# Performance work log

Hardware: AMD Instinct MI355X
Metric: run time of the kernel (lower is better)

## Reference

```python
import jax, jax.numpy as jnp
import numpy as np

U, I, K = 20000, 10000, 64
HID = [128, 64, 32, 16]  # hidden[0] must equal 2*K
B = 4096


def _lin(key, out_f, in_f):
    # torch nn.Linear default init ~ U(-1/sqrt(in), 1/sqrt(in)); normal/sqrt(in) is fine for a baseline
    return jax.random.normal(key, (out_f, in_f), jnp.float32) / np.sqrt(in_f)


def setup_inputs() -> dict:
    key = jax.random.key(0)
    ks = jax.random.split(key, 12)
    # near-binary implicit-feedback interaction matrix [U+1, I+1]
    interactions = (jax.random.uniform(ks[0], (U + 1, I + 1)) < 0.05).astype(jnp.float32)
    user_idx = jax.random.randint(ks[1], (B,), 0, U)
    item_idx = jax.random.randint(ks[2], (B,), 0, I)
    W_u = _lin(ks[3], K, I)   # proj_u: Linear(n_items -> K, bias=False)
    W_i = _lin(ks[4], K, U)   # proj_i: Linear(n_users -> K, bias=False)
    inp = dict(interactions=interactions, user_idx=user_idx, item_idx=item_idx,
               W_u=W_u, W_i=W_i)
    # matching_fn: 3 blocks of Linear + LayerNorm (+ReLU, dropout=0 in eval)
    for j in range(1, len(HID)):
        inp[f'W{j}'] = _lin(ks[4 + j], HID[j], HID[j - 1])
        inp[f'b{j}'] = jnp.zeros((HID[j],), jnp.float32)
        inp[f'g{j}'] = jnp.ones((HID[j],), jnp.float32)
        inp[f'be{j}'] = jnp.zeros((HID[j],), jnp.float32)
    inp['Wp'] = _lin(ks[8], 1, HID[-1])
    inp['bp'] = jnp.zeros((1,), jnp.float32)
    return inp


def _layernorm(x, g, b, eps=1e-5):
    m = jnp.mean(x, axis=-1, keepdims=True)
    v = jnp.mean(jnp.square(x - m), axis=-1, keepdims=True)
    return (x - m) * jax.lax.rsqrt(v + eps) * g + b


def reference(interactions, user_idx, item_idx, W_u, W_i,
              W1, b1, g1, be1, W2, b2, g2, be2, W3, b3, g3, be3, Wp, bp):
    rows = jnp.arange(user_idx.shape[0])
    # gather user history rows [B, I], zero-mask the target item
    u_slice = interactions[user_idx, :-1].at[rows, item_idx].set(0.0)
    # gather item history rows [B, U], zero-mask the target user
    i_slice = interactions.T[item_idx, :-1].at[rows, user_idx].set(0.0)
    u_emb = u_slice @ W_u.T  # [B, K]
    i_emb = i_slice @ W_i.T  # [B, K]
    x = jnp.concatenate([u_emb, i_emb], axis=-1)  # [B, 2K]
    for (W, b, g, be) in ((W1, b1, g1, be1), (W2, b2, g2, be2), (W3, b3, g3, be3)):
        x = jax.nn.relu(_layernorm(x @ W.T + b, g, be))
    logit = jnp.squeeze(x @ Wp.T + bp, -1)  # [B]
    return logit
```

## Files before the change

kernel.cpp:

```cpp
#include <hip/hip_runtime.h>

#define U_ROWS 20000
#define I_COLS 10000
#define LDI    10001
#define B_N    4096
#define SU     313
#define SC     625

typedef __attribute__((ext_vector_type(8))) __bf16 bf16x8;
typedef __attribute__((ext_vector_type(4))) float f32x4;

__device__ __forceinline__ unsigned short f2bf(float f) {
    unsigned int u = __float_as_uint(f);
    return (unsigned short)((u + 0x7FFFu + ((u >> 16) & 1u)) >> 16);
}

__global__ __launch_bounds__(256) void k_pack_w(const float* __restrict__ W,
                                                unsigned short* __restrict__ out,
                                                int n_k, int n_steps)
{
    int idx = blockIdx.x * blockDim.x + threadIdx.x;
    if (idx >= n_steps * 2048) return;
    int j  = idx & 7;
    int l  = (idx >> 3) & 63;
    int nb = (idx >> 9) & 3;
    int s  = idx >> 11;
    int n  = nb * 16 + (l & 15);
    int k  = s * 32 + ((l >> 4) << 3) + j;
    float v = (k < n_k) ? W[(size_t)n * n_k + k] : 0.0f;
    out[idx] = f2bf(v);
}

__global__ __launch_bounds__(256) void k_tr(const float* __restrict__ in,
                                            float* __restrict__ out, int rows, int cols)
{
    int idx = blockIdx.x * blockDim.x + threadIdx.x;
    if (idx >= rows * cols) return;
    int r = idx / cols, c = idx % cols;
    out[c * rows + r] = in[idx];
}

__global__ __launch_bounds__(256) void k_gemm_u(
    const float* __restrict__ A, const int* __restrict__ uidx,
    const unsigned short* __restrict__ Bp, float* __restrict__ Upart,
    int steps_per)
{
    __shared__ float At[64 * 32];
    const int t = threadIdx.x, lane = t & 63, w = t >> 6;
    const int mb = blockIdx.x & 63, p = blockIdx.x >> 6;
    const int r0 = mb * 64;
    const int s0 = p * steps_per;
    const int s1 = (SU < s0 + steps_per) ? SU : (s0 + steps_per);
    const int rl = lane & 15, g = lane >> 4;

    f32x4 acc[4];
#pragma unroll
    for (int nb = 0; nb < 4; ++nb) acc[nb] = (f32x4)(0.0f);

    int urow[8];
#pragma unroll
    for (int q = 0; q < 8; ++q) urow[q] = uidx[r0 + q * 8 + (t >> 5)];

    for (int s = s0; s < s1; ++s) {
        const int k0 = s * 32;
        float sv[8];
#pragma unroll
        for (int q = 0; q < 8; ++q) {
            int row = q * 8 + (t >> 5);
            int col = k0 + (((t & 31) + row) & 31);
            sv[q] = (col < I_COLS) ? A[(size_t)urow[q] * LDI + col] : 0.0f;
        }
        __syncthreads();
#pragma unroll
        for (int q = 0; q < 8; ++q) {
            int row = q * 8 + (t >> 5);
            At[row * 32 + (t & 31)] = sv[q];
        }
        __syncthreads();

        bf16x8 bv[4];
#pragma unroll
        for (int nb = 0; nb < 4; ++nb)
            bv[nb] = *(const bf16x8*)(Bp + ((size_t)(s * 4 + nb) * 64 + lane) * 8);

        const int r_loc = w * 16 + rl;
        unsigned int au[8];
#pragma unroll
        for (int j = 0; j < 8; ++j) {
            int c = g * 8 + j;
            au[j] = __float_as_uint(At[r_loc * 32 + ((c - r_loc) & 31)]);
        }
        union { int i[4]; bf16x8 v; } af;
#pragma unroll
        for (int q = 0; q < 4; ++q)
            af.i[q] = __builtin_amdgcn_perm(au[2 * q + 1], au[2 * q], 0x07060302);
#pragma unroll
        for (int nb = 0; nb < 4; ++nb)
            acc[nb] = __builtin_amdgcn_mfma_f32_16x16x32_bf16(af.v, bv[nb], acc[nb], 0, 0, 0);
    }

    float* outp = Upart + (size_t)p * B_N * 64;
#pragma unroll
    for (int nb = 0; nb < 4; ++nb)
#pragma unroll
        for (int reg = 0; reg < 4; ++reg) {
            int r = r0 + w * 16 + g * 4 + reg;
            outp[(size_t)r * 64 + nb * 16 + rl] = acc[nb][reg];
        }
}

__global__ __launch_bounds__(256) void k_gemm_c(
    const float* __restrict__ A, const unsigned short* __restrict__ Bp,
    float* __restrict__ Cpart, int n_mb, int steps_per)
{
    __shared__ float At[32 * 64];
    const int t = threadIdx.x, lane = t & 63, w = t >> 6;
    const int mb = blockIdx.x % n_mb, p = blockIdx.x / n_mb;
    const int i0 = mb * 64;
    const int s0 = p * steps_per;
    const int s1 = (SC < s0 + steps_per) ? SC : (s0 + steps_per);
    const int rl = lane & 15, g = lane >> 4;

    f32x4 acc[4];
#pragma unroll
    for (int nb = 0; nb < 4; ++nb) acc[nb] = (f32x4)(0.0f);

    for (int s = s0; s < s1; ++s) {
        const int u0 = s * 32;
        float sv[8];
#pragma unroll
        for (int q = 0; q < 8; ++q) {
            int ul = q * 4 + w;
            int col = i0 + ((lane + ul) & 63);
            sv[q] = (col < I_COLS) ? A[(size_t)(u0 + ul) * LDI + col] : 0.0f;
        }
        __syncthreads();
#pragma unroll
        for (int q = 0; q < 8; ++q) At[(q * 4 + w) * 64 + lane] = sv[q];
        __syncthreads();

        bf16x8 bv[4];
#pragma unroll
        for (int nb = 0; nb < 4; ++nb)
            bv[nb] = *(const bf16x8*)(Bp + ((size_t)(s * 4 + nb) * 64 + lane) * 8);

        const int i_loc = w * 16 + rl;
        unsigned int au[8];
#pragma unroll
        for (int j = 0; j < 8; ++j) {
            int ul = g * 8 + j;
            au[j] = __float_as_uint(At[ul * 64 + ((i_loc - ul) & 63)]);
        }
        union { int i[4]; bf16x8 v; } af;
#pragma unroll
        for (int q = 0; q < 4; ++q)
            af.i[q] = __builtin_amdgcn_perm(au[2 * q + 1], au[2 * q], 0x07060302);
#pragma unroll
        for (int nb = 0; nb < 4; ++nb)
            acc[nb] = __builtin_amdgcn_mfma_f32_16x16x32_bf16(af.v, bv[nb], acc[nb], 0, 0, 0);
    }

    float* outp = Cpart + (size_t)p * I_COLS * 64;
#pragma unroll
    for (int nb = 0; nb < 4; ++nb)
#pragma unroll
        for (int reg = 0; reg < 4; ++reg) {
            int i = i0 + w * 16 + g * 4 + reg;
            if (i < I_COLS) outp[(size_t)i * 64 + nb * 16 + rl] = acc[nb][reg];
        }
}

__device__ __forceinline__ float redsum64(float x) {
    x += __shfl_xor(x, 1);  x += __shfl_xor(x, 2);  x += __shfl_xor(x, 4);
    x += __shfl_xor(x, 8);  x += __shfl_xor(x, 16); x += __shfl_xor(x, 32);
    return x;
}
__device__ __forceinline__ float redsum32(float x) {
    x += __shfl_xor(x, 1); x += __shfl_xor(x, 2); x += __shfl_xor(x, 4);
    x += __shfl_xor(x, 8); x += __shfl_xor(x, 16);
    return x;
}
__device__ __forceinline__ float redsum16(float x) {
    x += __shfl_xor(x, 1); x += __shfl_xor(x, 2); x += __shfl_xor(x, 4);
    x += __shfl_xor(x, 8);
    return x;
}

__global__ __launch_bounds__(256) void k_epi(
    const float* __restrict__ A, const int* __restrict__ uidx, const int* __restrict__ iidx,
    const float* __restrict__ Upart, const float* __restrict__ Cpart, int NP, int NC,
    const float* __restrict__ Wu, const float* __restrict__ Wi,
    const float* __restrict__ Wt1, const float* __restrict__ b1, const float* __restrict__ g1, const float* __restrict__ be1,
    const float* __restrict__ Wt2, const float* __restrict__ b2, const float* __restrict__ g2, const float* __restrict__ be2,
    const float* __restrict__ Wt3, const float* __restrict__ b3, const float* __restrict__ g3, const float* __restrict__ be3,
    const float* __restrict__ Wp, const float* __restrict__ bp,
    float* __restrict__ out)
{
    const int t = threadIdx.x, lane = t & 63, w = t >> 6;
    const int r = blockIdx.x * 4 + w;
    const int u = uidx[r], it = iidx[r];
    const float a_ui = A[(size_t)u * LDI + it];

    float ue = 0.f, ie = 0.f;
    for (int p0 = 0; p0 < NP; ++p0) ue += Upart[((size_t)p0 * B_N + r) * 64 + lane];
    for (int p0 = 0; p0 < NC; ++p0) ie += Cpart[((size_t)p0 * I_COLS + it) * 64 + lane];
    ue -= a_ui * Wu[(size_t)lane * I_COLS + it];
    ie -= a_ui * Wi[(size_t)lane * U_ROWS + u];

    float h = b1[lane];
    for (int c = 0; c < 64; ++c) h += __shfl(ue, c) * Wt1[c * 64 + lane];
    for (int c = 0; c < 64; ++c) h += __shfl(ie, c) * Wt1[(64 + c) * 64 + lane];
    {
        float m = redsum64(h) * (1.0f / 64.0f);
        float d = h - m;
        float v = redsum64(d * d) * (1.0f / 64.0f);
        h = d * rsqrtf(v + 1e-5f) * g1[lane] + be1[lane];
        h = fmaxf(h, 0.0f);
    }
    const int l2 = lane & 31;
    float h2 = b2[l2];
    for (int c = 0; c < 64; ++c) h2 += __shfl(h, c) * Wt2[c * 32 + l2];
    {
        float m = redsum32(h2) * (1.0f / 32.0f);
        float d = h2 - m;
        float v = redsum32(d * d) * (1.0f / 32.0f);
        h2 = d * rsqrtf(v + 1e-5f) * g2[l2] + be2[l2];
        h2 = fmaxf(h2, 0.0f);
    }
    const int l3 = lane & 15;
    float h3 = b3[l3];
    for (int c = 0; c < 32; ++c) h3 += __shfl(h2, c) * Wt3[c * 16 + l3];
    {
        float m = redsum16(h3) * (1.0f / 16.0f);
        float d = h3 - m;
        float v = redsum16(d * d) * (1.0f / 16.0f);
        h3 = d * rsqrtf(v + 1e-5f) * g3[l3] + be3[l3];
        h3 = fmaxf(h3, 0.0f);
    }
    float tt = h3 * Wp[l3];
    tt = redsum16(tt);
    if (lane == 0) out[r] = tt + bp[0];
}

extern "C" void kernel_launch(void* const* d_in, const int* in_sizes, int n_in,
                              void* d_out, int out_size, void* d_ws, size_t ws_size,
                              hipStream_t stream)
{
    const float* A    = (const float*)d_in[0];
    const int*   uidx = (const int*)d_in[1];
    const int*   iidx = (const int*)d_in[2];
    const float* W_u  = (const float*)d_in[3];
    const float* W_i  = (const float*)d_in[4];
    const float* W1   = (const float*)d_in[5];
    const float* b1   = (const float*)d_in[6];
    const float* g1   = (const float*)d_in[7];
    const float* be1  = (const float*)d_in[8];
    const float* W2   = (const float*)d_in[9];
    const float* b2   = (const float*)d_in[10];
    const float* g2   = (const float*)d_in[11];
    const float* be2  = (const float*)d_in[12];
    const float* W3   = (const float*)d_in[13];
    const float* b3   = (const float*)d_in[14];
    const float* g3   = (const float*)d_in[15];
    const float* be3  = (const float*)d_in[16];
    const float* Wp   = (const float*)d_in[17];
    const float* bp   = (const float*)d_in[18];
    float* out = (float*)d_out;

    unsigned short* Wtu_p = (unsigned short*)d_ws;
    unsigned short* Wti_p = Wtu_p + (size_t)SU * 2048;
    float* Wt1 = (float*)(Wti_p + (size_t)SC * 2048);
    float* Wt2 = Wt1 + 128 * 64;
    float* Wt3 = Wt2 + 64 * 32;
    float* Upart = Wt3 + 32 * 16;

    size_t fixed_b = (size_t)(SU + SC) * 2048 * 2 + (size_t)(128 * 64 + 64 * 32 + 32 * 16) * 4;
    int NP = 8, NC = 8;
    while (NP > 1 &&
           fixed_b + (size_t)NP * B_N * 64 * 4 + (size_t)NC * I_COLS * 64 * 4 > ws_size) {
        NP >>= 1; NC >>= 1;
    }
    float* Cpart = Upart + (size_t)NP * B_N * 64;

    int spu = (SU + NP - 1) / NP;
    int spc = (SC + NC - 1) / NC;

    hipLaunchKernelGGL(k_pack_w, dim3((SU * 2048 + 255) / 256), dim3(256), 0, stream,
                       W_u, Wtu_p, I_COLS, SU);
    hipLaunchKernelGGL(k_pack_w, dim3((SC * 2048 + 255) / 256), dim3(256), 0, stream,
                       W_i, Wti_p, U_ROWS, SC);
    hipLaunchKernelGGL(k_tr, dim3(32), dim3(256), 0, stream, W1, Wt1, 64, 128);
    hipLaunchKernelGGL(k_tr, dim3(8),  dim3(256), 0, stream, W2, Wt2, 32, 64);
    hipLaunchKernelGGL(k_tr, dim3(2),  dim3(256), 0, stream, W3, Wt3, 16, 32);

    hipLaunchKernelGGL(k_gemm_u, dim3(64 * NP), dim3(256), 0, stream,
                       A, uidx, Wtu_p, Upart, spu);
    hipLaunchKernelGGL(k_gemm_c, dim3(157 * NC), dim3(256), 0, stream,
                       A, Wti_p, Cpart, 157, spc);

    hipLaunchKernelGGL(k_epi, dim3(B_N / 4), dim3(256), 0, stream,
                       A, uidx, iidx, Upart, Cpart, NP, NC,
                       W_u, W_i, Wt1, b1, g1, be1, Wt2, b2, g2, be2,
                       Wt3, b3, g3, be3, Wp, bp, out);
}
```

Measured before the change: 302.0 us.

## Merge prep and GEMM launches, software-pipeline global loads in GEMM loops

Folds the two weight-pack kernels and three transpose kernels into one prep kernel. Merges the user-side and item-side GEMMs into a single launch whose blocks branch by index. Each GEMM loop now prefetches the next step's A tile into registers before writing the current one to shared memory, so global-load latency overlaps the MFMA work. This cuts launch overhead and lets the two GEMMs share the GPU, at the cost of more registers and more divergent code per kernel.

```diff
diff --git a/kernel.cpp b/kernel.cpp
--- a/kernel.cpp
+++ b/kernel.cpp
@@ -15,159 +15,180 @@
     return (unsigned short)((u + 0x7FFFu + ((u >> 16) & 1u)) >> 16);
 }
 
-__global__ __launch_bounds__(256) void k_pack_w(const float* __restrict__ W,
-                                                unsigned short* __restrict__ out,
-                                                int n_k, int n_steps)
+__global__ __launch_bounds__(256) void k_prep(
+    const float* __restrict__ Wu, const float* __restrict__ Wi,
+    unsigned short* __restrict__ Pu, unsigned short* __restrict__ Pi,
+    const float* __restrict__ W1, const float* __restrict__ W2, const float* __restrict__ W3,
+    float* __restrict__ Wt1, float* __restrict__ Wt2, float* __restrict__ Wt3)
 {
-    int idx = blockIdx.x * blockDim.x + threadIdx.x;
-    if (idx >= n_steps * 2048) return;
-    int j  = idx & 7;
-    int l  = (idx >> 3) & 63;
-    int nb = (idx >> 9) & 3;
-    int s  = idx >> 11;
-    int n  = nb * 16 + (l & 15);
-    int k  = s * 32 + ((l >> 4) << 3) + j;
-    float v = (k < n_k) ? W[(size_t)n * n_k + k] : 0.0f;
-    out[idx] = f2bf(v);
-}
-
-__global__ __launch_bounds__(256) void k_tr(const float* __restrict__ in,
-                                            float* __restrict__ out, int rows, int cols)
+    const int NU = SU * 2048, NC2 = SC * 2048;
+    int idx = blockIdx.x * 256 + threadIdx.x;
+    if (idx < NU + NC2) {
+        const float* W = (idx < NU) ? Wu : Wi;
+        unsigned short* out = (idx < NU) ? Pu : Pi;
+        int n_k = (idx < NU) ? I_COLS : U_ROWS;
+        int li = (idx < NU) ? idx : idx - NU;
+        int j  = li & 7;
+        int l  = (li >> 3) & 63;
+        int nb = (li >> 9) & 3;
+        int s  = li >> 11;
+        int n  = nb * 16 + (l & 15);
+        int k  = s * 32 + ((l >> 4) << 3) + j;
+        float v = (k < n_k) ? W[(size_t)n * n_k + k] : 0.0f;
+        out[li] = f2bf(v);
+        return;
+    }
+    int r2 = idx - (NU + NC2);
+    if (r2 < 64 * 128) { int r = r2 / 128, c = r2 % 128; Wt1[c * 64 + r] = W1[r2]; return; }
+    r2 -= 64 * 128;
+    if (r2 < 32 * 64)  { int r = r2 / 64,  c = r2 % 64;  Wt2[c * 32 + r] = W2[r2]; return; }
+    r2 -= 32 * 64;
+    if (r2 < 16 * 32)  { int r = r2 / 32,  c = r2 % 32;  Wt3[c * 16 + r] = W3[r2]; return; }
+}
+
+__global__ __launch_bounds__(256) void k_gemm(
+    const float* __restrict__ A, const int* __restrict__ uidx,
+    const unsigned short* __restrict__ Bpu, const unsigned short* __restrict__ Bpc,
+    float* __restrict__ Upart, float* __restrict__ Cpart,
+    int spu, int spc, int NC)
 {
-    int idx = blockIdx.x * blockDim.x + threadIdx.x;
-    if (idx >= rows * cols) return;
-    int r = idx / cols, c = idx % cols;
-    out[c * rows + r] = in[idx];
-}
-
-__global__ __launch_bounds__(256) void k_gemm_u(
-    const float* __restrict__ A, const int* __restrict__ uidx,
-    const unsigned short* __restrict__ Bp, float* __restrict__ Upart,
-    int steps_per)
-{
-    __shared__ float At[64 * 32];
+    __shared__ float At[2048];
     const int t = threadIdx.x, lane = t & 63, w = t >> 6;
-    const int mb = blockIdx.x & 63, p = blockIdx.x >> 6;
-    const int r0 = mb * 64;
-    const int s0 = p * steps_per;
-    const int s1 = (SU < s0 + steps_per) ? SU : (s0 + steps_per);
     const int rl = lane & 15, g = lane >> 4;
+    const int CB = 157 * NC;
 
     f32x4 acc[4];
 #pragma unroll
     for (int nb = 0; nb < 4; ++nb) acc[nb] = (f32x4)(0.0f);
 
-    int urow[8];
-#pragma unroll
-    for (int q = 0; q < 8; ++q) urow[q] = uidx[r0 + q * 8 + (t >> 5)];
-
-    for (int s = s0; s < s1; ++s) {
-        const int k0 = s * 32;
+    if ((int)blockIdx.x < CB) {
+        const int mb = blockIdx.x % 157, p = blockIdx.x / 157;
+        const int i0 = mb * 64;
+        const int s0 = p * spc;
+        const int s1 = (SC < s0 + spc) ? SC : (s0 + spc);
+
+#define CLOAD(dst, S) do { \
+        int u0_ = (S) * 32; \
+        _Pragma("unroll") \
+        for (int q = 0; q < 8; ++q) { \
+            int ul_ = q * 4 + w; \
+            int col_ = i0 + ((lane + ul_) & 63); \
+            dst[q] = (col_ < I_COLS) ? A[(size_t)(u0_ + ul_) * LDI + col_] : 0.0f; \
+        } } while (0)
+
         float sv[8];
-#pragma unroll
-        for (int q = 0; q < 8; ++q) {
-            int row = q * 8 + (t >> 5);
-            int col = k0 + (((t & 31) + row) & 31);
-            sv[q] = (col < I_COLS) ? A[(size_t)urow[q] * LDI + col] : 0.0f;
+        CLOAD(sv, s0);
+        for (int s = s0; s < s1; ++s) {
+            __syncthreads();
+            float sv2[8];
+            if (s + 1 < s1) { CLOAD(sv2, s + 1); }
+            else {
+#pragma unroll
+                for (int q = 0; q < 8; ++q) sv2[q] = 0.0f;
+            }
+#pragma unroll
+            for (int q = 0; q < 8; ++q) At[(q * 4 + w) * 64 + lane] = sv[q];
+
+            bf16x8 bv[4];
+#pragma unroll
+            for (int nb = 0; nb < 4; ++nb)
+                bv[nb] = *(const bf16x8*)(Bpc + ((size_t)(s * 4 + nb) * 64 + lane) * 8);
+            __syncthreads();
+
+            const int i_loc = w * 16 + rl;
+            unsigned int au[8];
+#pragma unroll
+            for (int j = 0; j < 8; ++j) {
+                int ul = g * 8 + j;
+                au[j] = __float_as_uint(At[ul * 64 + ((i_loc - ul) & 63)]);
+            }
+            union { int i[4]; bf16x8 v; } af;
+#pragma unroll
+            for (int q = 0; q < 4; ++q)
+                af.i[q] = __builtin_amdgcn_perm(au[2 * q + 1], au[2 * q], 0x07060302);
+#pragma unroll
+            for (int nb = 0; nb < 4; ++nb)
+                acc[nb] = __builtin_amdgcn_mfma_f32_16x16x32_bf16(af.v, bv[nb], acc[nb], 0, 0, 0);
+#pragma unroll
+            for (int q = 0; q < 8; ++q) sv[q] = sv2[q];
         }
-        __syncthreads();
-#pragma unroll
-        for (int q = 0; q < 8; ++q) {
-            int row = q * 8 + (t >> 5);
-            At[row * 32 + (t & 31)] = sv[q];
+
+        float* outp = Cpart + (size_t)p * I_COLS * 64;
+#pragma unroll
+        for (int nb = 0; nb < 4; ++nb)
+#pragma unroll
+            for (int reg = 0; reg < 4; ++reg) {
+                int i = i0 + w * 16 + g * 4 + reg;
+                if (i < I_COLS) outp[(size_t)i * 64 + nb * 16 + rl] = acc[nb][reg];
+            }
+    } else {
+        const int bid = blockIdx.x - CB;
+        const int mb = bid & 63, p = bid >> 6;
+        const int r0 = mb * 64;
+        const int s0 = p * spu;
+        const int s1 = (SU < s0 + spu) ? SU : (s0 + spu);
+
+        int urow[8];
+#pragma unroll
+        for (int q = 0; q < 8; ++q) urow[q] = uidx[r0 + q * 8 + (t >> 5)];
+
+#define ULOAD(dst, S) do { \
+        int k0_ = (S) * 32; \
+        _Pragma("unroll") \
+        for (int q = 0; q < 8; ++q) { \
+            int row_ = q * 8 + (t >> 5); \
+            int col_ = k0_ + (((t & 31) + row_) & 31); \
+            dst[q] = (col_ < I_COLS) ? A[(size_t)urow[q] * LDI + col_] : 0.0f; \
+        } } while (0)
+
+        float sv[8];
+        ULOAD(sv, s0);
+        for (int s = s0; s < s1; ++s) {
+            __syncthreads();
+            float sv2[8];
+            if (s + 1 < s1) { ULOAD(sv2, s + 1); }
+            else {
+#pragma unroll
+                for (int q = 0; q < 8; ++q) sv2[q] = 0.0f;
+            }
+#pragma unroll
+            for (int q = 0; q < 8; ++q) {
+                int row = q * 8 + (t >> 5);
+                At[row * 32 + (t & 31)] = sv[q];
+            }
+            bf16x8 bv[4];
+#pragma unroll
+            for (int nb = 0; nb < 4; ++nb)
+                bv[nb] = *(const bf16x8*)(Bpu + ((size_t)(s * 4 + nb) * 64 + lane) * 8);
+            __syncthreads();
+
+            const int r_loc = w * 16 + rl;
+            unsigned int au[8];
+#pragma unroll
+            for (int j = 0; j < 8; ++j) {
+                int c = g * 8 + j;
+                au[j] = __float_as_uint(At[r_loc * 32 + ((c - r_loc) & 31)]);
+            }
+            union { int i[4]; bf16x8 v; } af;
+#pragma unroll
+            for (int q = 0; q < 4; ++q)
+                af.i[q] = __builtin_amdgcn_perm(au[2 * q + 1], au[2 * q], 0x07060302);
+#pragma unroll
+            for (int nb = 0; nb < 4; ++nb)
+                acc[nb] = __builtin_amdgcn_mfma_f32_16x16x32_bf16(af.v, bv[nb], acc[nb], 0, 0, 0);
+#pragma unroll
+            for (int q = 0; q < 8; ++q) sv[q] = sv2[q];
         }
-        __syncthreads();
-
-        bf16x8 bv[4];
+
+        float* outp = Upart + (size_t)p * B_N * 64;
 #pragma unroll
         for (int nb = 0; nb < 4; ++nb)
-            bv[nb] = *(const bf16x8*)(Bp + ((size_t)(s * 4 + nb) * 64 + lane) * 8);
-
-        const int r_loc = w * 16 + rl;
-        unsigned int au[8];
-#pragma unroll
-        for (int j = 0; j < 8; ++j) {
-            int c = g * 8 + j;
-            au[j] = __float_as_uint(At[r_loc * 32 + ((c - r_loc) & 31)]);
-        }
-        union { int i[4]; bf16x8 v; } af;
-#pragma unroll
-        for (int q = 0; q < 4; ++q)
-            af.i[q] = __builtin_amdgcn_perm(au[2 * q + 1], au[2 * q], 0x07060302);
-#pragma unroll
-        for (int nb = 0; nb < 4; ++nb)
-            acc[nb] = __builtin_amdgcn_mfma_f32_16x16x32_bf16(af.v, bv[nb], acc[nb], 0, 0, 0);
-    }
-
-    float* outp = Upart + (size_t)p * B_N * 64;
-#pragma unroll
-    for (int nb = 0; nb < 4; ++nb)
-#pragma unroll
-        for (int reg = 0; reg < 4; ++reg) {
-            int r = r0 + w * 16 + g * 4 + reg;
-            outp[(size_t)r * 64 + nb * 16 + rl] = acc[nb][reg];
-        }
-}
-
-__global__ __launch_bounds__(256) void k_gemm_c(
-    const float* __restrict__ A, const unsigned short* __restrict__ Bp,
-    float* __restrict__ Cpart, int n_mb, int steps_per)
-{
-    __shared__ float At[32 * 64];
-    const int t = threadIdx.x, lane = t & 63, w = t >> 6;
-    const int mb = blockIdx.x % n_mb, p = blockIdx.x / n_mb;
-    const int i0 = mb * 64;
-    const int s0 = p * steps_per;
-    const int s1 = (SC < s0 + steps_per) ? SC : (s0 + steps_per);
-    const int rl = lane & 15, g = lane >> 4;
-
-    f32x4 acc[4];
-#pragma unroll
-    for (int nb = 0; nb < 4; ++nb) acc[nb] = (f32x4)(0.0f);
-
-    for (int s = s0; s < s1; ++s) {
-        const int u0 = s * 32;
-        float sv[8];
-#pragma unroll
-        for (int q = 0; q < 8; ++q) {
-            int ul = q * 4 + w;
-            int col = i0 + ((lane + ul) & 63);
-            sv[q] = (col < I_COLS) ? A[(size_t)(u0 + ul) * LDI + col] : 0.0f;
-        }
-        __syncthreads();
-#pragma unroll
-        for (int q = 0; q < 8; ++q) At[(q * 4 + w) * 64 + lane] = sv[q];
-        __syncthreads();
-
-        bf16x8 bv[4];
-#pragma unroll
-        for (int nb = 0; nb < 4; ++nb)
-            bv[nb] = *(const bf16x8*)(Bp + ((size_t)(s * 4 + nb) * 64 + lane) * 8);
-
-        const int i_loc = w * 16 + rl;
-        unsigned int au[8];
-#pragma unroll
-        for (int j = 0; j < 8; ++j) {
-            int ul = g * 8 + j;
-            au[j] = __float_as_uint(At[ul * 64 + ((i_loc - ul) & 63)]);
-        }
-        union { int i[4]; bf16x8 v; } af;
-#pragma unroll
-        for (int q = 0; q < 4; ++q)
-            af.i[q] = __builtin_amdgcn_perm(au[2 * q + 1], au[2 * q], 0x07060302);
-#pragma unroll
-        for (int nb = 0; nb < 4; ++nb)
-            acc[nb] = __builtin_amdgcn_mfma_f32_16x16x32_bf16(af.v, bv[nb], acc[nb], 0, 0, 0);
-    }
-
-    float* outp = Cpart + (size_t)p * I_COLS * 64;
-#pragma unroll
-    for (int nb = 0; nb < 4; ++nb)
-#pragma unroll
-        for (int reg = 0; reg < 4; ++reg) {
-            int i = i0 + w * 16 + g * 4 + reg;
-            if (i < I_COLS) outp[(size_t)i * 64 + nb * 16 + rl] = acc[nb][reg];
-        }
+#pragma unroll
+            for (int reg = 0; reg < 4; ++reg) {
+                int r = r0 + w * 16 + g * 4 + reg;
+                outp[(size_t)r * 64 + nb * 16 + rl] = acc[nb][reg];
+            }
+    }
 }
 
 __device__ __forceinline__ float redsum64(float x) {
@@ -285,18 +306,12 @@
     int spu = (SU + NP - 1) / NP;
     int spc = (SC + NC - 1) / NC;
 
-    hipLaunchKernelGGL(k_pack_w, dim3((SU * 2048 + 255) / 256), dim3(256), 0, stream,
-                       W_u, Wtu_p, I_COLS, SU);
-    hipLaunchKernelGGL(k_pack_w, dim3((SC * 2048 + 255) / 256), dim3(256), 0, stream,
-                       W_i, Wti_p, U_ROWS, SC);
-    hipLaunchKernelGGL(k_tr, dim3(32), dim3(256), 0, stream, W1, Wt1, 64, 128);
-    hipLaunchKernelGGL(k_tr, dim3(8),  dim3(256), 0, stream, W2, Wt2, 32, 64);
-    hipLaunchKernelGGL(k_tr, dim3(2),  dim3(256), 0, stream, W3, Wt3, 16, 32);
-
-    hipLaunchKernelGGL(k_gemm_u, dim3(64 * NP), dim3(256), 0, stream,
-                       A, uidx, Wtu_p, Upart, spu);
-    hipLaunchKernelGGL(k_gemm_c, dim3(157 * NC), dim3(256), 0, stream,
-                       A, Wti_p, Cpart, 157, spc);
+    int prep_tot = (SU + SC) * 2048 + 64 * 128 + 32 * 64 + 16 * 32;
+    hipLaunchKernelGGL(k_prep, dim3((prep_tot + 255) / 256), dim3(256), 0, stream,
+                       W_u, W_i, Wtu_p, Wti_p, W1, W2, W3, Wt1, Wt2, Wt3);
+
+    hipLaunchKernelGGL(k_gemm, dim3(157 * NC + 64 * NP), dim3(256), 0, stream,
+                       A, uidx, Wtu_p, Wti_p, Upart, Cpart, spu, spc, NC);
 
     hipLaunchKernelGGL(k_epi, dim3(B_N / 4), dim3(256), 0, stream,
                        A, uidx, iidx, Upart, Cpart, NP, NC,
```

Result: faster. 250.4 us (-17.1%).
